# Kernel tuning notes

Measured on AMD Instinct MI355X. Metric: run time of the kernel, lower is better.

## Reference

```python
import jax, jax.numpy as jnp
import numpy as np

EMBED_DIM = 1024
N_HEADS = 16
HEAD_DIM = EMBED_DIM // N_HEADS


def setup_inputs() -> dict:
    key = jax.random.key(0)
    k_x, k_wi, k_bi, k_wo, k_bo = jax.random.split(key, 5)
    B, N, C = 4, 2048, EMBED_DIM
    scale = 1.0 / np.sqrt(C)
    return {
        "x": jax.random.normal(k_x, (B, N, C), dtype=jnp.float32),
        "w_in": jax.random.normal(k_wi, (C, 3 * C), dtype=jnp.float32) * scale,
        "b_in": jax.random.normal(k_bi, (3 * C,), dtype=jnp.float32) * 0.01,
        "w_out": jax.random.normal(k_wo, (C, C), dtype=jnp.float32) * scale,
        "b_out": jax.random.normal(k_bo, (C,), dtype=jnp.float32) * 0.01,
    }


def reference(x, w_in, b_in, w_out, b_out):
    B, N, C = x.shape
    H, D = N_HEADS, HEAD_DIM
    qkv = x @ w_in + b_in  # (B, N, 3C)
    q, k, v = jnp.split(qkv, 3, axis=-1)
    # (B, H, N, D)
    q = q.reshape(B, N, H, D).transpose(0, 2, 1, 3)
    k = k.reshape(B, N, H, D).transpose(0, 2, 1, 3)
    v = v.reshape(B, N, H, D).transpose(0, 2, 1, 3)
    # Naive attention: full (B,H,N,N) scores, NO sqrt(d) scaling (as in source)
    scores = jnp.einsum("bhnd,bhmd->bhnm", q, k)
    attn = jax.nn.softmax(scores, axis=-1)
    out = jnp.einsum("bhnm,bhmd->bhnd", attn, v)
    out = out.transpose(0, 2, 1, 3).reshape(B, N, C)
    return out @ w_out + b_out
```

## Files before the change

### kernel.cpp

```cpp
#include <hip/hip_runtime.h>
#include <hip/hip_bf16.h>
#include <stdint.h>

typedef __attribute__((ext_vector_type(8))) __bf16 bf8v;
typedef __attribute__((ext_vector_type(4))) float f4v;

#define L2E 1.44269504088896f

__device__ __forceinline__ unsigned short f2bf(float f) {
  union { float f; unsigned u; } v; v.f = f;
  unsigned r = v.u + 0x7fffu + ((v.u >> 16) & 1u);
  return (unsigned short)(r >> 16);
}

__device__ __forceinline__ unsigned pk2bf(float f0, float f1) {
  union { __hip_bfloat162 h; unsigned u; } c;
  c.h = __float22bfloat162_rn(make_float2(f0, f1));
  return c.u;
}

__device__ __forceinline__ float exp2_hw(float x) {
  return __builtin_amdgcn_exp2f(x);
}

__device__ __forceinline__ void gl_lds16(const void* g, void* l) {
  __builtin_amdgcn_global_load_lds(
      (__attribute__((address_space(1))) void*)(g),
      (__attribute__((address_space(3))) void*)(l), 16, 0, 0);
}

__global__ void cast_bf16_kernel(const float* __restrict__ in,
                                 unsigned short* __restrict__ out) {
  int i = blockIdx.x * 256 + threadIdx.x;
  float4 v = ((const float4*)in)[i];
  ushort4 o;
  o.x = f2bf(v.x); o.y = f2bf(v.y); o.z = f2bf(v.z); o.w = f2bf(v.w);
  ((ushort4*)out)[i] = o;
}

__global__ void transpose_w_kernel(const float* __restrict__ w_in,
                                   const float* __restrict__ w_out,
                                   unsigned short* __restrict__ wiT,
                                   unsigned short* __restrict__ woT) {
  __shared__ float tile[32][33];
  int bx = blockIdx.x;
  const float* in; unsigned short* out; int C, c0;
  if (bx < 96) { in = w_in;  out = wiT; C = 3072; c0 = bx * 32; }
  else         { in = w_out; out = woT; C = 1024; c0 = (bx - 96) * 32; }
  int r0 = blockIdx.y * 32;
  int tx = threadIdx.x, ty = threadIdx.y;
#pragma unroll
  for (int j = 0; j < 4; ++j)
    tile[ty + 8 * j][tx] = in[(size_t)(r0 + ty + 8 * j) * C + c0 + tx];
  __syncthreads();
#pragma unroll
  for (int j = 0; j < 4; ++j)
    out[(size_t)(c0 + ty + 8 * j) * 1024 + r0 + tx] = f2bf(tile[tx][ty + 8 * j]);
}

__global__ void transpose_v_kernel(const unsigned short* __restrict__ qkv,
                                   unsigned short* __restrict__ vtg) {
  __shared__ unsigned short tile[32][33];
  int bh = blockIdx.z;
  int d0 = blockIdx.y * 32;
  int n0 = blockIdx.x * 32;
  int b = bh >> 4, h = bh & 15;
  int tx = threadIdx.x, ty = threadIdx.y;
  const unsigned short* src = qkv + (size_t)b * 2048 * 3072 + 2048 + h * 64 + d0;
#pragma unroll
  for (int j = 0; j < 4; ++j)
    tile[ty + 8 * j][tx] = src[(size_t)(n0 + ty + 8 * j) * 3072 + tx];
  __syncthreads();
  unsigned short* dst = vtg + ((size_t)bh * 64) * 2048;
#pragma unroll
  for (int j = 0; j < 4; ++j)
    dst[(size_t)(d0 + ty + 8 * j) * 2048 + n0 + tx] = tile[tx][ty + 8 * j];
}

__global__ __launch_bounds__(512, 2) void gemm_bt256(
    const unsigned short* __restrict__ A,
    const unsigned short* __restrict__ BT,
    const float* __restrict__ bias,
    unsigned short* __restrict__ C,
    int N, int K, int nbx, int scale_ncols, float scale) {
  __shared__ __align__(16) unsigned short As[2][256 * 64];
  __shared__ __align__(16) unsigned short Bs[2][256 * 64];
  const int tid = threadIdx.x;
  const int wave = tid >> 6, lane = tid & 63;
  const int lo = lane & 15, hi = lane >> 4;
  const int wm = wave >> 2, wn = wave & 3;

  const int nwg = gridDim.x;
  const int cpx = nwg >> 3;
  const int s = (blockIdx.x & 7) * cpx + (blockIdx.x >> 3);
  const int by = s / nbx, bx = s - by * nbx;
  const int m0 = by * 256, n0 = bx * 256;

  const int srow = lane >> 3;
  const int scol = ((lane & 7) * 8) ^ ((lane >> 1) & 16);
  const unsigned short* gA = A + (size_t)(m0 + wave * 8 + srow) * K + scol;
  const unsigned short* gB = BT + (size_t)(n0 + wave * 8 + srow) * K + scol;

  const int colsw0 = (hi * 8) ^ ((lo & 4) << 2);
  const int colsw1 = (32 + hi * 8) ^ ((lo & 4) << 2);
  const int rA = wm * 128 + lo;
  const int rB = wn * 64 + lo;

  f4v acc[8][4] = {};
  const int nt = K >> 6;

#pragma unroll
  for (int j = 0; j < 4; ++j) {
    gl_lds16(gA + (size_t)(j * 64) * K, &As[0][(j * 64 + wave * 8) * 64]);
    gl_lds16(gB + (size_t)(j * 64) * K, &Bs[0][(j * 64 + wave * 8) * 64]);
  }

  for (int t = 0; t < nt; ++t) {
    const int c = t & 1;
    __builtin_amdgcn_s_barrier();
    __builtin_amdgcn_sched_barrier(0);
    if (t + 1 < nt) {
      const unsigned short* gA1 = gA + (size_t)(t + 1) * 64;
      const unsigned short* gB1 = gB + (size_t)(t + 1) * 64;
#pragma unroll
      for (int j = 0; j < 4; ++j) {
        gl_lds16(gA1 + (size_t)(j * 64) * K, &As[c ^ 1][(j * 64 + wave * 8) * 64]);
        gl_lds16(gB1 + (size_t)(j * 64) * K, &Bs[c ^ 1][(j * 64 + wave * 8) * 64]);
      }
      asm volatile("s_waitcnt vmcnt(8)" ::: "memory");
    } else {
      asm volatile("s_waitcnt vmcnt(0)" ::: "memory");
    }
    __builtin_amdgcn_sched_barrier(0);
    __builtin_amdgcn_s_barrier();
    __builtin_amdgcn_sched_barrier(0);

    bf8v b[4][2];
#pragma unroll
    for (int fn = 0; fn < 4; ++fn) {
      b[fn][0] = *(const bf8v*)&Bs[c][(rB + fn * 16) * 64 + colsw0];
      b[fn][1] = *(const bf8v*)&Bs[c][(rB + fn * 16) * 64 + colsw1];
    }
#pragma unroll
    for (int p = 0; p < 4; ++p) {
      bf8v a[2][2];
#pragma unroll
      for (int i = 0; i < 2; ++i) {
        a[i][0] = *(const bf8v*)&As[c][(rA + (p * 2 + i) * 16) * 64 + colsw0];
        a[i][1] = *(const bf8v*)&As[c][(rA + (p * 2 + i) * 16) * 64 + colsw1];
      }
      __builtin_amdgcn_s_setprio(1);
#pragma unroll
      for (int ks = 0; ks < 2; ++ks)
#pragma unroll
        for (int i = 0; i < 2; ++i)
#pragma unroll
          for (int fn = 0; fn < 4; ++fn)
            acc[p * 2 + i][fn] = __builtin_amdgcn_mfma_f32_16x16x32_bf16(
                a[i][ks], b[fn][ks], acc[p * 2 + i][fn], 0, 0, 0);
      __builtin_amdgcn_s_setprio(0);
    }
  }

#pragma unroll
  for (int i = 0; i < 8; ++i) {
#pragma unroll
    for (int r = 0; r < 4; ++r) {
      int row = m0 + wm * 128 + i * 16 + hi * 4 + r;
#pragma unroll
      for (int j = 0; j < 4; ++j) {
        int col = n0 + wn * 64 + j * 16 + lo;
        float v = acc[i][j][r] + bias[col];
        if (col < scale_ncols) v *= scale;
        C[(size_t)row * N + col] = f2bf(v);
      }
    }
  }
}

__global__ __launch_bounds__(256, 4) void gemm_bt_sm(
    const unsigned short* __restrict__ A,
    const unsigned short* __restrict__ BT,
    const float* __restrict__ bias,
    float* __restrict__ C,
    int M, int N, int K) {
  __shared__ __align__(16) unsigned short As[64 * 32];
  __shared__ __align__(16) unsigned short Bs[128 * 32];
  const int tid = threadIdx.x;
  const int wave = tid >> 6, lane = tid & 63;
  const int lo = lane & 15, hi = lane >> 4;
  const int m0 = blockIdx.y * 64, n0 = blockIdx.x * 128;
  const int wm = (wave >> 1) * 32, wn = (wave & 1) * 64;

  f4v acc[2][4] = {};

  const int srow = lane >> 2;
  const int scol = (lane & 3) * 8;

  for (int k0 = 0; k0 < K; k0 += 32) {
    gl_lds16(A + (size_t)(m0 + wave * 16 + srow) * K + k0 + scol,
             &As[(wave * 16) * 32]);
#pragma unroll
    for (int p = 0; p < 2; ++p) {
      int r = p * 64 + wave * 16 + srow;
      gl_lds16(BT + (size_t)(n0 + r) * K + k0 + scol,
               &Bs[(p * 64 + wave * 16) * 32]);
    }
    __syncthreads();
    bf8v a[2], b[4];
#pragma unroll
    for (int i = 0; i < 2; ++i)
      a[i] = *(const bf8v*)&As[(wm + i * 16 + lo) * 32 + hi * 8];
#pragma unroll
    for (int j = 0; j < 4; ++j)
      b[j] = *(const bf8v*)&Bs[(wn + j * 16 + lo) * 32 + hi * 8];
#pragma unroll
    for (int i = 0; i < 2; ++i)
#pragma unroll
      for (int j = 0; j < 4; ++j)
        acc[i][j] = __builtin_amdgcn_mfma_f32_16x16x32_bf16(a[i], b[j], acc[i][j], 0, 0, 0);
    __syncthreads();
  }

#pragma unroll
  for (int i = 0; i < 2; ++i) {
#pragma unroll
    for (int r = 0; r < 4; ++r) {
      int row = m0 + wm + i * 16 + hi * 4 + r;
#pragma unroll
      for (int j = 0; j < 4; ++j) {
        int col = n0 + wn + j * 16 + lo;
        C[(size_t)row * N + col] = acc[i][j][r] + bias[col];
      }
    }
  }
}

#define FSTR 72

__global__ __launch_bounds__(256, 4) void flash_attn(
    const unsigned short* __restrict__ qkv,
    const unsigned short* __restrict__ vtg,
    unsigned short* __restrict__ y) {
  __shared__ __align__(16) unsigned short Ps[128 * FSTR];
  __shared__ __align__(16) unsigned short Kt[64 * FSTR];
  __shared__ __align__(16) unsigned short Vt[64 * FSTR];
  const int tid = threadIdx.x;
  const int wave = tid >> 6, lane = tid & 63;
  const int lo = lane & 15, hi = lane >> 4;

  const int lin = (((blockIdx.z << 4) | blockIdx.y) << 4) | blockIdx.x;
  const int swz = (lin & 7) * 128 + (lin >> 3);
  const int q0 = (swz & 15) << 7;
  const int h  = (swz >> 4) & 15;
  const int b  = swz >> 8;

  const size_t base = (size_t)b * 2048 * 3072;
  const int qoff = h * 64, koff = 1024 + h * 64;
  const unsigned short* vsrc = vtg + (size_t)(b * 16 + h) * 64 * 2048;

  const int m_st = tid >> 3, c_st = tid & 7;
  const unsigned short* kg = qkv + base + koff;
  float4 rk0, rk1, rv0, rv1;
  auto kv_load = [&](int kt) {
    const int mb = kt * 64;
    rk0 = *(const float4*)(kg + (size_t)(mb + m_st) * 3072 + c_st * 8);
    rk1 = *(const float4*)(kg + (size_t)(mb + m_st + 32) * 3072 + c_st * 8);
    rv0 = *(const float4*)(vsrc + (size_t)m_st * 2048 + mb + c_st * 8);
    rv1 = *(const float4*)(vsrc + (size_t)(m_st + 32) * 2048 + mb + c_st * 8);
  };
  auto kv_write = [&]() {
    *(float4*)&Kt[m_st * FSTR + c_st * 8] = rk0;
    *(float4*)&Kt[(m_st + 32) * FSTR + c_st * 8] = rk1;
    *(float4*)&Vt[m_st * FSTR + c_st * 8] = rv0;
    *(float4*)&Vt[(m_st + 32) * FSTR + c_st * 8] = rv1;
  };

  kv_load(0);

#pragma unroll
  for (int i = 0; i < 4; ++i) {
    int cid = i * 256 + tid;
    int m = cid >> 3, c = cid & 7;
    *(float4*)&Ps[m * FSTR + c * 8] =
        *(const float4*)(qkv + base + (size_t)(q0 + m) * 3072 + qoff + c * 8);
  }
  __syncthreads();
  bf8v bq[2][2];
#pragma unroll
  for (int qt = 0; qt < 2; ++qt)
#pragma unroll
    for (int ks = 0; ks < 2; ++ks)
      bq[qt][ks] = *(const bf8v*)&Ps[(wave * 32 + qt * 16 + lo) * FSTR + ks * 32 + hi * 8];

  f4v O[2][4] = {};
  f4v acc_l[2] = {};
  union { bf8v v; unsigned short u[8]; } onesu;
#pragma unroll
  for (int i = 0; i < 8; ++i) onesu.u[i] = 0x3F80;
  const bf8v ones = onesu.v;

  for (int kt = 0; kt < 32; ++kt) {
    asm volatile("" ::: "memory");
    __builtin_amdgcn_s_barrier();
    asm volatile("" ::: "memory");
    kv_write();
    if (kt < 31) kv_load(kt + 1);
    asm volatile("s_waitcnt lgkmcnt(0)" ::: "memory");
    __builtin_amdgcn_s_barrier();
    asm volatile("" ::: "memory");

#pragma unroll
    for (int ct = 0; ct < 4; ++ct) {
      f4v s0 = {}, s1 = {};
      __builtin_amdgcn_s_setprio(1);
#pragma unroll
      for (int ks = 0; ks < 2; ++ks) {
        bf8v ak = *(const bf8v*)&Kt[(ct * 16 + lo) * FSTR + ks * 32 + hi * 8];
        s0 = __builtin_amdgcn_mfma_f32_16x16x32_bf16(ak, bq[0][ks], s0, 0, 0, 0);
        s1 = __builtin_amdgcn_mfma_f32_16x16x32_bf16(ak, bq[1][ks], s1, 0, 0, 0);
      }
      __builtin_amdgcn_s_setprio(0);
      {
        float p0 = exp2_hw(s0[0]), p1 = exp2_hw(s0[1]);
        float p2 = exp2_hw(s0[2]), p3 = exp2_hw(s0[3]);
        uint2 w; w.x = pk2bf(p0, p1); w.y = pk2bf(p2, p3);
        *(uint2*)&Ps[(wave * 32 + lo) * FSTR + ct * 16 + hi * 4] = w;
      }
      {
        float p0 = exp2_hw(s1[0]), p1 = exp2_hw(s1[1]);
        float p2 = exp2_hw(s1[2]), p3 = exp2_hw(s1[3]);
        uint2 w; w.x = pk2bf(p0, p1); w.y = pk2bf(p2, p3);
        *(uint2*)&Ps[(wave * 32 + 16 + lo) * FSTR + ct * 16 + hi * 4] = w;
      }
    }

#pragma unroll
    for (int ks = 0; ks < 2; ++ks) {
      bf8v ap0 = *(const bf8v*)&Ps[(wave * 32 + lo) * FSTR + ks * 32 + hi * 8];
      bf8v ap1 = *(const bf8v*)&Ps[(wave * 32 + 16 + lo) * FSTR + ks * 32 + hi * 8];
      __builtin_amdgcn_s_setprio(1);
      acc_l[0] = __builtin_amdgcn_mfma_f32_16x16x32_bf16(ap0, ones, acc_l[0], 0, 0, 0);
      acc_l[1] = __builtin_amdgcn_mfma_f32_16x16x32_bf16(ap1, ones, acc_l[1], 0, 0, 0);
#pragma unroll
      for (int dt = 0; dt < 4; ++dt) {
        bf8v bv = *(const bf8v*)&Vt[(dt * 16 + lo) * FSTR + ks * 32 + hi * 8];
        O[0][dt] = __builtin_amdgcn_mfma_f32_16x16x32_bf16(ap0, bv, O[0][dt], 0, 0, 0);
        O[1][dt] = __builtin_amdgcn_mfma_f32_16x16x32_bf16(ap1, bv, O[1][dt], 0, 0, 0);
      }
      __builtin_amdgcn_s_setprio(0);
    }
  }

#pragma unroll
  for (int qt = 0; qt < 2; ++qt) {
#pragma unroll
    for (int r = 0; r < 4; ++r) {
      float inv = 1.f / acc_l[qt][r];
      int row = q0 + wave * 32 + qt * 16 + hi * 4 + r;
      size_t orow = ((size_t)b * 2048 + row) * 1024 + h * 64;
#pragma unroll
      for (int dt = 0; dt < 4; ++dt)
        y[orow + dt * 16 + lo] = f2bf(O[qt][dt][r] * inv);
    }
  }
}

extern "C" void kernel_launch(void* const* d_in, const int* in_sizes, int n_in,
                              void* d_out, int out_size, void* d_ws, size_t ws_size,
                              hipStream_t stream) {
  (void)in_sizes; (void)n_in; (void)out_size; (void)ws_size;
  const float* x     = (const float*)d_in[0];
  const float* w_in  = (const float*)d_in[1];
  const float* b_in  = (const float*)d_in[2];
  const float* w_out = (const float*)d_in[3];
  const float* b_out = (const float*)d_in[4];

  unsigned short* xb  = (unsigned short*)d_ws;
  unsigned short* wiT = xb  + (size_t)8192 * 1024;
  unsigned short* woT = wiT + (size_t)3072 * 1024;
  unsigned short* qkv = woT + (size_t)1024 * 1024;
  unsigned short* yb  = qkv + (size_t)8192 * 3072;
  unsigned short* vtg = xb;

  cast_bf16_kernel<<<8192, 256, 0, stream>>>(x, xb);
  transpose_w_kernel<<<dim3(128, 32), dim3(32, 8), 0, stream>>>(w_in, w_out, wiT, woT);

  gemm_bt256<<<384, 512, 0, stream>>>(xb, wiT, b_in, qkv, 3072, 1024, 12, 1024, L2E);
  transpose_v_kernel<<<dim3(64, 2, 64), dim3(32, 8), 0, stream>>>(qkv, vtg);
  flash_attn<<<dim3(16, 16, 4), 256, 0, stream>>>(qkv, vtg, yb);
  gemm_bt_sm<<<dim3(8, 128), 256, 0, stream>>>(yb, woT, b_out, (float*)d_out,
                                               8192, 1024, 1024);
}
```

Before: 303.2 us.

## Double flash-attention query tile per block and merge prep kernels

Each flash-attention block now handles 256 query rows instead of 128, with each wave owning 64 rows. Every K/V tile loaded into LDS is therefore reused across twice as many queries, halving K/V global traffic and barrier count per query. The price is more registers (launch bounds lowered to 2 blocks), a larger LDS footprint and only 512 blocks. The bf16 cast of x and the weight transposes are also merged into a single launch to save launch overhead.

```diff
diff --git a/kernel.cpp b/kernel.cpp
--- a/kernel.cpp
+++ b/kernel.cpp
@@ -29,26 +29,29 @@
       (__attribute__((address_space(3))) void*)(l), 16, 0, 0);
 }
 
-__global__ void cast_bf16_kernel(const float* __restrict__ in,
-                                 unsigned short* __restrict__ out) {
-  int i = blockIdx.x * 256 + threadIdx.x;
-  float4 v = ((const float4*)in)[i];
-  ushort4 o;
-  o.x = f2bf(v.x); o.y = f2bf(v.y); o.z = f2bf(v.z); o.w = f2bf(v.w);
-  ((ushort4*)out)[i] = o;
-}
-
-__global__ void transpose_w_kernel(const float* __restrict__ w_in,
-                                   const float* __restrict__ w_out,
-                                   unsigned short* __restrict__ wiT,
-                                   unsigned short* __restrict__ woT) {
+__global__ void prep_kernel(const float* __restrict__ x,
+                            const float* __restrict__ w_in,
+                            const float* __restrict__ w_out,
+                            unsigned short* __restrict__ xb,
+                            unsigned short* __restrict__ wiT,
+                            unsigned short* __restrict__ woT) {
   __shared__ float tile[32][33];
   int bx = blockIdx.x;
+  if (bx < 8192) {
+    int i = bx * 256 + threadIdx.x;
+    float4 v = ((const float4*)x)[i];
+    ushort4 o;
+    o.x = f2bf(v.x); o.y = f2bf(v.y); o.z = f2bf(v.z); o.w = f2bf(v.w);
+    ((ushort4*)xb)[i] = o;
+    return;
+  }
+  int idx = bx - 8192;
+  int bxx = idx & 127, byy = idx >> 7;
   const float* in; unsigned short* out; int C, c0;
-  if (bx < 96) { in = w_in;  out = wiT; C = 3072; c0 = bx * 32; }
-  else         { in = w_out; out = woT; C = 1024; c0 = (bx - 96) * 32; }
-  int r0 = blockIdx.y * 32;
-  int tx = threadIdx.x, ty = threadIdx.y;
+  if (bxx < 96) { in = w_in;  out = wiT; C = 3072; c0 = bxx * 32; }
+  else          { in = w_out; out = woT; C = 1024; c0 = (bxx - 96) * 32; }
+  int r0 = byy * 32;
+  int tx = threadIdx.x & 31, ty = threadIdx.x >> 5;
 #pragma unroll
   for (int j = 0; j < 4; ++j)
     tile[ty + 8 * j][tx] = in[(size_t)(r0 + ty + 8 * j) * C + c0 + tx];
@@ -238,22 +241,22 @@
 
 #define FSTR 72
 
-__global__ __launch_bounds__(256, 4) void flash_attn(
+__global__ __launch_bounds__(256, 2) void flash_attn(
     const unsigned short* __restrict__ qkv,
     const unsigned short* __restrict__ vtg,
     unsigned short* __restrict__ y) {
-  __shared__ __align__(16) unsigned short Ps[128 * FSTR];
+  __shared__ __align__(16) unsigned short Ps[256 * FSTR];
   __shared__ __align__(16) unsigned short Kt[64 * FSTR];
   __shared__ __align__(16) unsigned short Vt[64 * FSTR];
   const int tid = threadIdx.x;
   const int wave = tid >> 6, lane = tid & 63;
   const int lo = lane & 15, hi = lane >> 4;
 
-  const int lin = (((blockIdx.z << 4) | blockIdx.y) << 4) | blockIdx.x;
-  const int swz = (lin & 7) * 128 + (lin >> 3);
-  const int q0 = (swz & 15) << 7;
-  const int h  = (swz >> 4) & 15;
-  const int b  = swz >> 8;
+  const int lin = blockIdx.x;
+  const int swz = (lin & 7) * 64 + (lin >> 3);
+  const int q0 = (swz & 7) << 8;
+  const int h  = (swz >> 3) & 15;
+  const int b  = swz >> 7;
 
   const size_t base = (size_t)b * 2048 * 3072;
   const int qoff = h * 64, koff = 1024 + h * 64;
@@ -279,22 +282,22 @@
   kv_load(0);
 
 #pragma unroll
-  for (int i = 0; i < 4; ++i) {
+  for (int i = 0; i < 8; ++i) {
     int cid = i * 256 + tid;
     int m = cid >> 3, c = cid & 7;
     *(float4*)&Ps[m * FSTR + c * 8] =
         *(const float4*)(qkv + base + (size_t)(q0 + m) * 3072 + qoff + c * 8);
   }
   __syncthreads();
-  bf8v bq[2][2];
-#pragma unroll
-  for (int qt = 0; qt < 2; ++qt)
+  bf8v bq[4][2];
+#pragma unroll
+  for (int qt = 0; qt < 4; ++qt)
 #pragma unroll
     for (int ks = 0; ks < 2; ++ks)
-      bq[qt][ks] = *(const bf8v*)&Ps[(wave * 32 + qt * 16 + lo) * FSTR + ks * 32 + hi * 8];
-
-  f4v O[2][4] = {};
-  f4v acc_l[2] = {};
+      bq[qt][ks] = *(const bf8v*)&Ps[(wave * 64 + qt * 16 + lo) * FSTR + ks * 32 + hi * 8];
+
+  f4v O[4][4] = {};
+  f4v acc_l[4] = {};
   union { bf8v v; unsigned short u[8]; } onesu;
 #pragma unroll
   for (int i = 0; i < 8; ++i) onesu.u[i] = 0x3F80;
@@ -312,52 +315,52 @@
 
 #pragma unroll
     for (int ct = 0; ct < 4; ++ct) {
-      f4v s0 = {}, s1 = {};
+      f4v s[4] = {{}, {}, {}, {}};
       __builtin_amdgcn_s_setprio(1);
 #pragma unroll
       for (int ks = 0; ks < 2; ++ks) {
         bf8v ak = *(const bf8v*)&Kt[(ct * 16 + lo) * FSTR + ks * 32 + hi * 8];
-        s0 = __builtin_amdgcn_mfma_f32_16x16x32_bf16(ak, bq[0][ks], s0, 0, 0, 0);
-        s1 = __builtin_amdgcn_mfma_f32_16x16x32_bf16(ak, bq[1][ks], s1, 0, 0, 0);
+#pragma unroll
+        for (int qt = 0; qt < 4; ++qt)
+          s[qt] = __builtin_amdgcn_mfma_f32_16x16x32_bf16(ak, bq[qt][ks], s[qt], 0, 0, 0);
       }
       __builtin_amdgcn_s_setprio(0);
-      {
-        float p0 = exp2_hw(s0[0]), p1 = exp2_hw(s0[1]);
-        float p2 = exp2_hw(s0[2]), p3 = exp2_hw(s0[3]);
+#pragma unroll
+      for (int qt = 0; qt < 4; ++qt) {
+        float p0 = exp2_hw(s[qt][0]), p1 = exp2_hw(s[qt][1]);
+        float p2 = exp2_hw(s[qt][2]), p3 = exp2_hw(s[qt][3]);
         uint2 w; w.x = pk2bf(p0, p1); w.y = pk2bf(p2, p3);
-        *(uint2*)&Ps[(wave * 32 + lo) * FSTR + ct * 16 + hi * 4] = w;
-      }
-      {
-        float p0 = exp2_hw(s1[0]), p1 = exp2_hw(s1[1]);
-        float p2 = exp2_hw(s1[2]), p3 = exp2_hw(s1[3]);
-        uint2 w; w.x = pk2bf(p0, p1); w.y = pk2bf(p2, p3);
-        *(uint2*)&Ps[(wave * 32 + 16 + lo) * FSTR + ct * 16 + hi * 4] = w;
+        *(uint2*)&Ps[(wave * 64 + qt * 16 + lo) * FSTR + ct * 16 + hi * 4] = w;
       }
     }
 
 #pragma unroll
     for (int ks = 0; ks < 2; ++ks) {
-      bf8v ap0 = *(const bf8v*)&Ps[(wave * 32 + lo) * FSTR + ks * 32 + hi * 8];
-      bf8v ap1 = *(const bf8v*)&Ps[(wave * 32 + 16 + lo) * FSTR + ks * 32 + hi * 8];
+      bf8v ap[4];
+#pragma unroll
+      for (int qt = 0; qt < 4; ++qt)
+        ap[qt] = *(const bf8v*)&Ps[(wave * 64 + qt * 16 + lo) * FSTR + ks * 32 + hi * 8];
       __builtin_amdgcn_s_setprio(1);
-      acc_l[0] = __builtin_amdgcn_mfma_f32_16x16x32_bf16(ap0, ones, acc_l[0], 0, 0, 0);
-      acc_l[1] = __builtin_amdgcn_mfma_f32_16x16x32_bf16(ap1, ones, acc_l[1], 0, 0, 0);
+#pragma unroll
+      for (int qt = 0; qt < 4; ++qt)
+        acc_l[qt] = __builtin_amdgcn_mfma_f32_16x16x32_bf16(ap[qt], ones, acc_l[qt], 0, 0, 0);
 #pragma unroll
       for (int dt = 0; dt < 4; ++dt) {
         bf8v bv = *(const bf8v*)&Vt[(dt * 16 + lo) * FSTR + ks * 32 + hi * 8];
-        O[0][dt] = __builtin_amdgcn_mfma_f32_16x16x32_bf16(ap0, bv, O[0][dt], 0, 0, 0);
-        O[1][dt] = __builtin_amdgcn_mfma_f32_16x16x32_bf16(ap1, bv, O[1][dt], 0, 0, 0);
+#pragma unroll
+        for (int qt = 0; qt < 4; ++qt)
+          O[qt][dt] = __builtin_amdgcn_mfma_f32_16x16x32_bf16(ap[qt], bv, O[qt][dt], 0, 0, 0);
       }
       __builtin_amdgcn_s_setprio(0);
     }
   }
 
 #pragma unroll
-  for (int qt = 0; qt < 2; ++qt) {
+  for (int qt = 0; qt < 4; ++qt) {
 #pragma unroll
     for (int r = 0; r < 4; ++r) {
       float inv = 1.f / acc_l[qt][r];
-      int row = q0 + wave * 32 + qt * 16 + hi * 4 + r;
+      int row = q0 + wave * 64 + qt * 16 + hi * 4 + r;
       size_t orow = ((size_t)b * 2048 + row) * 1024 + h * 64;
 #pragma unroll
       for (int dt = 0; dt < 4; ++dt)
@@ -383,12 +386,11 @@
   unsigned short* yb  = qkv + (size_t)8192 * 3072;
   unsigned short* vtg = xb;
 
-  cast_bf16_kernel<<<8192, 256, 0, stream>>>(x, xb);
-  transpose_w_kernel<<<dim3(128, 32), dim3(32, 8), 0, stream>>>(w_in, w_out, wiT, woT);
+  prep_kernel<<<12288, 256, 0, stream>>>(x, w_in, w_out, xb, wiT, woT);
 
   gemm_bt256<<<384, 512, 0, stream>>>(xb, wiT, b_in, qkv, 3072, 1024, 12, 1024, L2E);
   transpose_v_kernel<<<dim3(64, 2, 64), dim3(32, 8), 0, stream>>>(qkv, vtg);
-  flash_attn<<<dim3(16, 16, 4), 256, 0, stream>>>(qkv, vtg, yb);
+  flash_attn<<<512, 256, 0, stream>>>(qkv, vtg, yb);
   gemm_bt_sm<<<dim3(8, 128), 256, 0, stream>>>(yb, woT, b_out, (float*)d_out,
                                                8192, 1024, 1024);
 }
```

New measurement: 294.4 us. 1.03x faster.
